# Kernel optimization log

Hardware: AMD Instinct MI355X
Metric: run time of the kernel (lower is better)

## Reference

```python
import jax, jax.numpy as jnp
import numpy as np

N = 50000      # nodes
E = 600000     # edges
D = 128        # hidden_dim (bottleneck=1)
G = 64         # graphs in batch
GN_EPS = 1e-5  # GraphNorm eps


def setup_inputs() -> dict:
    key = jax.random.key(0)
    ks = jax.random.split(key, 10)
    node_h = jax.random.normal(ks[0], (N, D), dtype=jnp.float32)
    edge_attr = jax.random.normal(ks[1], (E, D), dtype=jnp.float32)
    batch = jnp.sort(jax.random.randint(ks[2], (N,), 0, G)).astype(jnp.int64)
    edge_index = jax.random.randint(ks[3], (2, E), 0, N).astype(jnp.int64)
    # params: lin1, conv.lin (edge linear), conv.eps, GraphNorm(weight,bias,mean_scale)
    w1 = jax.random.normal(ks[4], (D, D), dtype=jnp.float32) * 0.02
    b1 = jnp.zeros((D,), dtype=jnp.float32)
    we = jax.random.normal(ks[5], (D, D), dtype=jnp.float32) * 0.02
    be = jnp.zeros((D,), dtype=jnp.float32)
    eps = jnp.zeros((), dtype=jnp.float32)  # train_eps, init 0
    gn_weight = jnp.ones((D,), dtype=jnp.float32)
    gn_bias = jnp.zeros((D,), dtype=jnp.float32)
    gn_mean_scale = jnp.ones((D,), dtype=jnp.float32)
    return {"node_h": node_h, "edge_attr": edge_attr, "batch": batch,
            "edge_index": edge_index, "w1": w1, "b1": b1, "we": we, "be": be,
            "eps": eps, "gn_weight": gn_weight, "gn_bias": gn_bias,
            "gn_mean_scale": gn_mean_scale}


def graph_norm(x, batch, weight, bias, mean_scale):
    ones = jnp.ones((x.shape[0],), dtype=x.dtype)
    cnt = jnp.maximum(jax.ops.segment_sum(ones, batch, num_segments=G), 1.0)[:, None]
    mean = jax.ops.segment_sum(x, batch, num_segments=G) / cnt
    out = x - mean[batch] * mean_scale
    var = jax.ops.segment_sum(out * out, batch, num_segments=G) / cnt
    std = jnp.sqrt(var + GN_EPS)
    return weight * out / std[batch] + bias


def reference(node_h, edge_attr, batch, edge_index, w1, b1, we, be, eps,
              gn_weight, gn_bias, gn_mean_scale):
    h = node_h @ w1.T + b1                                  # lin1: [N, D]
    src, dst = edge_index[0], edge_index[1]
    # GINEConvMod message: SiLU(x_j + lin(edge_attr)); gather -> add -> act
    msg = jax.nn.silu(h[src] + (edge_attr @ we.T + be))     # [E, D]
    agg = jax.ops.segment_sum(msg, dst, num_segments=N)     # scatter-add
    conv = (1.0 + eps) * h + agg                            # nn = Identity
    # dropout(p=0) and lin2=Identity are no-ops
    out = jax.nn.silu(conv)
    return graph_norm(out + node_h, batch, gn_weight, gn_bias, gn_mean_scale)
```

## Files before the change

kernel.cpp:

```cpp
#include <hip/hip_runtime.h>
#include <hip/hip_bf16.h>

#define NN 50000
#define NE 600000
#define DIM 128
#define NG 64
#define NCHUNK 98

using bf16x8 = __attribute__((ext_vector_type(8))) __bf16;
using f32x4  = __attribute__((ext_vector_type(4))) float;

__device__ __forceinline__ bf16x8 cvt8(const float* __restrict__ p) {
    f32x4 a = *(const f32x4*)p;
    f32x4 b = *(const f32x4*)(p + 4);
    bf16x8 r;
    #pragma unroll
    for (int i = 0; i < 4; ++i) { r[i] = (__bf16)a[i]; r[i + 4] = (__bf16)b[i]; }
    return r;
}

__device__ __forceinline__ void stage_weights(const float* __restrict__ W, __bf16* sW) {
    for (int i = threadIdx.x; i < 128 * 16; i += 256) {
        int row = i >> 4, seg = i & 15;
        *(bf16x8*)(&sW[row * 136 + seg * 8]) = cvt8(W + row * 128 + seg * 8);
    }
    __syncthreads();
}

__global__ __launch_bounds__(256) void gemm_bias(
    const float* __restrict__ X, const float* __restrict__ W,
    const float* __restrict__ bias, float* __restrict__ Y, int M)
{
    __shared__ __bf16 sW[128 * 136];
    stage_weights(W, sW);

    int wave = threadIdx.x >> 6, lane = threadIdx.x & 63;
    int col = lane & 15, quad = lane >> 4;
    int tile = (blockIdx.x * 4 + wave) * 16;
    if (tile >= M) return;

    f32x4 acc[8] = {};
    const float* xp = X + (size_t)(tile + col) * DIM + quad * 8;
    #pragma unroll
    for (int k0 = 0; k0 < 128; k0 += 32) {
        bf16x8 a = cvt8(xp + k0);
        #pragma unroll
        for (int t = 0; t < 8; ++t) {
            bf16x8 b = *(const bf16x8*)(&sW[(t * 16 + col) * 136 + k0 + quad * 8]);
            acc[t] = __builtin_amdgcn_mfma_f32_16x16x32_bf16(a, b, acc[t], 0, 0, 0);
        }
    }
    float bv[8];
    #pragma unroll
    for (int t = 0; t < 8; ++t) bv[t] = bias[t * 16 + col];
    #pragma unroll
    for (int r = 0; r < 4; ++r) {
        float* yp = Y + (size_t)(tile + quad * 4 + r) * DIM;
        #pragma unroll
        for (int t = 0; t < 8; ++t) yp[t * 16 + col] = acc[t][r] + bv[t];
    }
}

__global__ __launch_bounds__(256) void k_hist(const int* __restrict__ dst, int* __restrict__ deg) {
    int e = blockIdx.x * 256 + threadIdx.x;
    if (e < NE) atomicAdd(&deg[dst[e]], 1);
}

__global__ __launch_bounds__(256) void k_scan_a(const int* __restrict__ deg, int* __restrict__ chunkSum) {
    __shared__ int s[256];
    int c = blockIdx.x, t = threadIdx.x;
    int b = c * 512 + t;
    int v = (b < NN) ? deg[b] : 0;
    if (b + 256 < NN) v += deg[b + 256];
    s[t] = v; __syncthreads();
    for (int off = 128; off > 0; off >>= 1) {
        if (t < off) s[t] += s[t + off];
        __syncthreads();
    }
    if (t == 0) chunkSum[c] = s[0];
}

__global__ __launch_bounds__(128) void k_scan_b(const int* __restrict__ chunkSum,
                                                int* __restrict__ chunkOff, int* __restrict__ rowptr) {
    __shared__ int s[128];
    int t = threadIdx.x;
    int v = (t < NCHUNK) ? chunkSum[t] : 0;
    s[t] = v; __syncthreads();
    for (int off = 1; off < 128; off <<= 1) {
        int x = (t >= off) ? s[t - off] : 0;
        __syncthreads();
        s[t] += x;
        __syncthreads();
    }
    chunkOff[t] = s[t] - v;
    if (t == 0) rowptr[NN] = NE;
}

__global__ __launch_bounds__(512) void k_scan_c(const int* __restrict__ deg,
                                                const int* __restrict__ chunkOff,
                                                int* __restrict__ rowptr, int* __restrict__ pos) {
    __shared__ int s[512];
    int c = blockIdx.x, t = threadIdx.x;
    int i = c * 512 + t;
    int v = (i < NN) ? deg[i] : 0;
    s[t] = v; __syncthreads();
    for (int off = 1; off < 512; off <<= 1) {
        int x = (t >= off) ? s[t - off] : 0;
        __syncthreads();
        s[t] += x;
        __syncthreads();
    }
    if (i < NN) { rowptr[i] = chunkOff[c] + s[t] - v; pos[i] = 0; }
}

__global__ __launch_bounds__(256) void k_slot(const int* __restrict__ dst,
                                              const int* __restrict__ rowptr,
                                              int* __restrict__ pos, int* __restrict__ slot) {
    int e = blockIdx.x * 256 + threadIdx.x;
    if (e >= NE) return;
    int d = dst[e];
    int p = atomicAdd(&pos[d], 1);
    slot[e] = rowptr[d] + p;
}

__global__ __launch_bounds__(256) void edge_msg_sorted(
    const float* __restrict__ EA, const float* __restrict__ W,
    const float* __restrict__ bias,
    const int* __restrict__ src, const int* __restrict__ slot,
    const float* __restrict__ H, __hip_bfloat16* __restrict__ MSG)
{
    __shared__ __bf16 sW[128 * 136];
    stage_weights(W, sW);

    int wave = threadIdx.x >> 6, lane = threadIdx.x & 63;
    int col = lane & 15, quad = lane >> 4;
    int tile = (blockIdx.x * 4 + wave) * 16;

    f32x4 acc[8] = {};
    const float* xp = EA + (size_t)(tile + col) * DIM + quad * 8;
    #pragma unroll
    for (int k0 = 0; k0 < 128; k0 += 32) {
        bf16x8 a = cvt8(xp + k0);
        #pragma unroll
        for (int t = 0; t < 8; ++t) {
            bf16x8 b = *(const bf16x8*)(&sW[(t * 16 + col) * 136 + k0 + quad * 8]);
            acc[t] = __builtin_amdgcn_mfma_f32_16x16x32_bf16(a, b, acc[t], 0, 0, 0);
        }
    }
    float bv[8];
    #pragma unroll
    for (int t = 0; t < 8; ++t) bv[t] = bias[t * 16 + col];

    #pragma unroll
    for (int r = 0; r < 4; ++r) {
        int e = tile + quad * 4 + r;
        int s  = src[e];
        int sl = slot[e];
        const float* hp = H + (size_t)s * DIM;
        __hip_bfloat16* mp = MSG + (size_t)sl * DIM;
        #pragma unroll
        for (int t = 0; t < 8; ++t) {
            int d = t * 16 + col;
            float v = acc[t][r] + bv[t] + hp[d];
            v = v / (1.f + __expf(-v));
            mp[d] = __float2bfloat16(v);
        }
    }
}

__global__ __launch_bounds__(128) void k_gather(
    const __hip_bfloat16* __restrict__ MSG, const int* __restrict__ rowptr,
    float* __restrict__ H, const float* __restrict__ node_h,
    const float* __restrict__ epsp)
{
    int n = blockIdx.x, d = threadIdx.x;
    int s = rowptr[n], epos = rowptr[n + 1];
    float acc = 0.f;
    for (int e = s; e < epos; ++e)
        acc += __bfloat162float(MSG[(size_t)e * DIM + d]);
    size_t idx = (size_t)n * DIM + d;
    float v = (1.f + epsp[0]) * H[idx] + acc;
    v = v / (1.f + __expf(-v));
    H[idx] = v + node_h[idx];
}

__global__ __launch_bounds__(128) void stats_pass(
    const float* __restrict__ X, const int* __restrict__ batch,
    float* __restrict__ SUMS, float* __restrict__ CNT, int npb)
{
    int d = threadIdx.x;
    int n0 = blockIdx.x * npb;
    int nend = min(n0 + npb, NN);
    if (n0 >= NN) return;
    int cur_g = batch[n0];
    float run = 0.f; int runlen = 0;
    for (int n = n0; n < nend; ++n) {
        int g = batch[n];
        if (g != cur_g) {
            atomicAdd(&SUMS[cur_g * DIM + d], run);
            if (d == 0) atomicAdd(&CNT[cur_g], (float)runlen);
            run = 0.f; runlen = 0; cur_g = g;
        }
        run += X[(size_t)n * DIM + d]; runlen++;
    }
    atomicAdd(&SUMS[cur_g * DIM + d], run);
    if (d == 0) atomicAdd(&CNT[cur_g], (float)runlen);
}

__global__ __launch_bounds__(128) void var_pass(
    const float* __restrict__ X, const int* __restrict__ batch,
    const float* __restrict__ msc,
    const float* __restrict__ SUMS, const float* __restrict__ CNT,
    float* __restrict__ VARS, int npb)
{
    int d = threadIdx.x;
    int n0 = blockIdx.x * npb;
    int nend = min(n0 + npb, NN);
    if (n0 >= NN) return;
    float ms = msc[d];
    int cur_g = batch[n0];
    float c = fmaxf(CNT[cur_g], 1.f);
    float mean = SUMS[cur_g * DIM + d] / c;
    float run = 0.f;
    for (int n = n0; n < nend; ++n) {
        int g = batch[n];
        if (g != cur_g) {
            atomicAdd(&VARS[cur_g * DIM + d], run);
            run = 0.f; cur_g = g;
            c = fmaxf(CNT[g], 1.f);
            mean = SUMS[g * DIM + d] / c;
        }
        float v = X[(size_t)n * DIM + d] - mean * ms;
        run += v * v;
    }
    atomicAdd(&VARS[cur_g * DIM + d], run);
}

__global__ __launch_bounds__(128) void finalize(
    const float* __restrict__ X, const int* __restrict__ batch,
    const float* __restrict__ msc,
    const float* __restrict__ SUMS, const float* __restrict__ VARS,
    const float* __restrict__ CNT,
    const float* __restrict__ gw, const float* __restrict__ gb,
    float* __restrict__ OUT, int npb)
{
    int d = threadIdx.x;
    int n0 = blockIdx.x * npb;
    int nend = min(n0 + npb, NN);
    if (n0 >= NN) return;
    float ms = msc[d], wd = gw[d], bd = gb[d];
    int cur_g = -1;
    float mean = 0.f, rstd = 0.f;
    for (int n = n0; n < nend; ++n) {
        int g = batch[n];
        if (g != cur_g) {
            cur_g = g;
            float c = fmaxf(CNT[g], 1.f);
            mean = SUMS[g * DIM + d] / c;
            rstd = rsqrtf(VARS[g * DIM + d] / c + 1e-5f);
        }
        size_t idx = (size_t)n * DIM + d;
        float v = X[idx] - mean * ms;
        OUT[idx] = wd * v * rstd + bd;
    }
}

__global__ __launch_bounds__(256) void edge_msg_atomic(
    const float* __restrict__ EA, const float* __restrict__ W,
    const float* __restrict__ bias,
    const int* __restrict__ src, const int* __restrict__ dst,
    const float* __restrict__ H, float* __restrict__ AGG)
{
    __shared__ __bf16 sW[128 * 136];
    stage_weights(W, sW);
    int wave = threadIdx.x >> 6, lane = threadIdx.x & 63;
    int col = lane & 15, quad = lane >> 4;
    int tile = (blockIdx.x * 4 + wave) * 16;
    f32x4 acc[8] = {};
    const float* xp = EA + (size_t)(tile + col) * DIM + quad * 8;
    #pragma unroll
    for (int k0 = 0; k0 < 128; k0 += 32) {
        bf16x8 a = cvt8(xp + k0);
        #pragma unroll
        for (int t = 0; t < 8; ++t) {
            bf16x8 b = *(const bf16x8*)(&sW[(t * 16 + col) * 136 + k0 + quad * 8]);
            acc[t] = __builtin_amdgcn_mfma_f32_16x16x32_bf16(a, b, acc[t], 0, 0, 0);
        }
    }
    float bv[8];
    #pragma unroll
    for (int t = 0; t < 8; ++t) bv[t] = bias[t * 16 + col];
    #pragma unroll
    for (int r = 0; r < 4; ++r) {
        int e = tile + quad * 4 + r;
        int s = src[e], dd = dst[e];
        const float* hp = H + (size_t)s * DIM;
        float* ap = AGG + (size_t)dd * DIM;
        #pragma unroll
        for (int t = 0; t < 8; ++t) {
            int d = t * 16 + col;
            float v = acc[t][r] + bv[t] + hp[d];
            v = v / (1.f + __expf(-v));
            atomicAdd(&ap[d], v);
        }
    }
}

__global__ __launch_bounds__(128) void fuse_x_atomic(
    float* __restrict__ H, const float* __restrict__ AGG,
    const float* __restrict__ node_h, const float* __restrict__ epsp, int npb)
{
    int d = threadIdx.x;
    int n0 = blockIdx.x * npb;
    int nend = min(n0 + npb, NN);
    if (n0 >= NN) return;
    float epsv = 1.f + epsp[0];
    for (int n = n0; n < nend; ++n) {
        size_t idx = (size_t)n * DIM + d;
        float v = epsv * H[idx] + AGG[idx];
        v = v / (1.f + __expf(-v));
        H[idx] = v + node_h[idx];
    }
}

extern "C" void kernel_launch(void* const* d_in, const int* in_sizes, int n_in,
                              void* d_out, int out_size, void* d_ws, size_t ws_size,
                              hipStream_t stream) {
    const float* node_h    = (const float*)d_in[0];
    const float* edge_attr = (const float*)d_in[1];
    const int*   batch     = (const int*)d_in[2];
    const int*   eidx      = (const int*)d_in[3];
    const float* w1        = (const float*)d_in[4];
    const float* b1        = (const float*)d_in[5];
    const float* we        = (const float*)d_in[6];
    const float* be        = (const float*)d_in[7];
    const float* eps       = (const float*)d_in[8];
    const float* gnw       = (const float*)d_in[9];
    const float* gnb       = (const float*)d_in[10];
    const float* gnms      = (const float*)d_in[11];
    const int* src = eidx, * dst = eidx + NE;

    char* base = (char*)d_ws;
    float* H = (float*)base;

    size_t oMSG   = 25600000;
    size_t oROW   = oMSG + 153600000;
    size_t oDEG   = oROW + 200064;
    size_t oSUMS  = oDEG + 200000;
    size_t oVARS  = oSUMS + 32768;
    size_t oCNT   = oVARS + 32768;
    size_t oSLOT  = oCNT + 256;
    size_t oCSA   = oSLOT + 2400000;
    size_t oCSB   = oCSA + 512;
    size_t needed = oCSB + 512;

    bool fast = ws_size >= needed;

    if (fast) {
        __hip_bfloat16* MSG = (__hip_bfloat16*)(base + oMSG);
        int* rowptr = (int*)(base + oROW);
        int* deg    = (int*)(base + oDEG);
        float* SUMS = (float*)(base + oSUMS);
        float* VARS = (float*)(base + oVARS);
        float* CNT  = (float*)(base + oCNT);
        int* slot   = (int*)(base + oSLOT);
        int* csum   = (int*)(base + oCSA);
        int* coff   = (int*)(base + oCSB);

        hipMemsetAsync(deg, 0, 200000 + 32768 + 32768 + 256, stream);

        gemm_bias<<<782, 256, 0, stream>>>(node_h, w1, b1, H, NN);
        k_hist  <<<(NE + 255) / 256, 256, 0, stream>>>(dst, deg);
        k_scan_a<<<NCHUNK, 256, 0, stream>>>(deg, csum);
        k_scan_b<<<1, 128, 0, stream>>>(csum, coff, rowptr);
        k_scan_c<<<NCHUNK, 512, 0, stream>>>(deg, coff, rowptr, deg );
        k_slot  <<<(NE + 255) / 256, 256, 0, stream>>>(dst, rowptr, deg, slot);
        edge_msg_sorted<<<9375, 256, 0, stream>>>(edge_attr, we, be, src, slot, H, MSG);
        k_gather<<<NN, 128, 0, stream>>>(MSG, rowptr, H, node_h, eps);
        stats_pass<<<3125, 128, 0, stream>>>(H, batch, SUMS, CNT, 16);
        var_pass  <<<3125, 128, 0, stream>>>(H, batch, gnms, SUMS, CNT, VARS, 16);
        finalize  <<<3125, 128, 0, stream>>>(H, batch, gnms, SUMS, VARS, CNT, gnw, gnb,
                                             (float*)d_out, 16);
    } else {
        float* AGG  = H + 6400000;
        float* SUMS = H + 12800000;
        float* VARS = SUMS + NG * DIM;
        float* CNT  = VARS + NG * DIM;
        hipMemsetAsync(AGG, 0, (size_t)(6400000 + NG * DIM * 2 + NG) * sizeof(float), stream);
        gemm_bias<<<782, 256, 0, stream>>>(node_h, w1, b1, H, NN);
        edge_msg_atomic<<<9375, 256, 0, stream>>>(edge_attr, we, be, src, dst, H, AGG);
        fuse_x_atomic<<<3125, 128, 0, stream>>>(H, AGG, node_h, eps, 16);
        stats_pass<<<3125, 128, 0, stream>>>(H, batch, SUMS, CNT, 16);
        var_pass  <<<3125, 128, 0, stream>>>(H, batch, gnms, SUMS, CNT, VARS, 16);
        finalize  <<<3125, 128, 0, stream>>>(H, batch, gnms, SUMS, VARS, CNT, gnw, gnb,
                                             (float*)d_out, 16);
    }
}
```

Measured before the change: 725.9 us.

## Transpose MFMA operands for row-contiguous epilogues and fuse GraphNorm variance pass

Swaps the A/B operands of the MFMA so each lane holds four contiguous output columns of one row. Epilogues can then use vectorized f32x4 bias and H loads and f32x4 or bf16x4 stores, with one src/slot lookup per lane instead of four scattered ones. The gather loop is unrolled by four with independent accumulators. GraphNorm variance now comes from a single-pass sum of squares, E[x^2] - mean^2*ms*(2-ms), which drops one full read of H but is less numerically robust than the two-pass form.

```diff
diff --git a/kernel.cpp b/kernel.cpp
--- a/kernel.cpp
+++ b/kernel.cpp
@@ -8,6 +8,7 @@
 #define NCHUNK 98
 
 using bf16x8 = __attribute__((ext_vector_type(8))) __bf16;
+using bf16x4 = __attribute__((ext_vector_type(4))) __bf16;
 using f32x4  = __attribute__((ext_vector_type(4))) float;
 
 __device__ __forceinline__ bf16x8 cvt8(const float* __restrict__ p) {
@@ -43,21 +44,21 @@
     const float* xp = X + (size_t)(tile + col) * DIM + quad * 8;
     #pragma unroll
     for (int k0 = 0; k0 < 128; k0 += 32) {
-        bf16x8 a = cvt8(xp + k0);
+        bf16x8 b = cvt8(xp + k0);
         #pragma unroll
         for (int t = 0; t < 8; ++t) {
-            bf16x8 b = *(const bf16x8*)(&sW[(t * 16 + col) * 136 + k0 + quad * 8]);
+            bf16x8 a = *(const bf16x8*)(&sW[(t * 16 + col) * 136 + k0 + quad * 8]);
             acc[t] = __builtin_amdgcn_mfma_f32_16x16x32_bf16(a, b, acc[t], 0, 0, 0);
         }
     }
-    float bv[8];
-    #pragma unroll
-    for (int t = 0; t < 8; ++t) bv[t] = bias[t * 16 + col];
-    #pragma unroll
-    for (int r = 0; r < 4; ++r) {
-        float* yp = Y + (size_t)(tile + quad * 4 + r) * DIM;
-        #pragma unroll
-        for (int t = 0; t < 8; ++t) yp[t * 16 + col] = acc[t][r] + bv[t];
+    float* yp = Y + (size_t)(tile + col) * DIM + quad * 4;
+    #pragma unroll
+    for (int t = 0; t < 8; ++t) {
+        f32x4 bv = *(const f32x4*)(bias + t * 16 + quad * 4);
+        f32x4 o;
+        #pragma unroll
+        for (int r = 0; r < 4; ++r) o[r] = acc[t][r] + bv[r];
+        *(f32x4*)(yp + t * 16) = o;
     }
 }
 
@@ -140,31 +141,31 @@
     const float* xp = EA + (size_t)(tile + col) * DIM + quad * 8;
     #pragma unroll
     for (int k0 = 0; k0 < 128; k0 += 32) {
-        bf16x8 a = cvt8(xp + k0);
+        bf16x8 b = cvt8(xp + k0);
         #pragma unroll
         for (int t = 0; t < 8; ++t) {
-            bf16x8 b = *(const bf16x8*)(&sW[(t * 16 + col) * 136 + k0 + quad * 8]);
+            bf16x8 a = *(const bf16x8*)(&sW[(t * 16 + col) * 136 + k0 + quad * 8]);
             acc[t] = __builtin_amdgcn_mfma_f32_16x16x32_bf16(a, b, acc[t], 0, 0, 0);
         }
     }
-    float bv[8];
-    #pragma unroll
-    for (int t = 0; t < 8; ++t) bv[t] = bias[t * 16 + col];
-
-    #pragma unroll
-    for (int r = 0; r < 4; ++r) {
-        int e = tile + quad * 4 + r;
-        int s  = src[e];
-        int sl = slot[e];
-        const float* hp = H + (size_t)s * DIM;
-        __hip_bfloat16* mp = MSG + (size_t)sl * DIM;
-        #pragma unroll
-        for (int t = 0; t < 8; ++t) {
-            int d = t * 16 + col;
-            float v = acc[t][r] + bv[t] + hp[d];
+
+    int e  = tile + col;
+    int s  = src[e];
+    int sl = slot[e];
+    const float* hp = H + (size_t)s * DIM + quad * 4;
+    __hip_bfloat16* mp = MSG + (size_t)sl * DIM + quad * 4;
+    #pragma unroll
+    for (int t = 0; t < 8; ++t) {
+        f32x4 bv = *(const f32x4*)(bias + t * 16 + quad * 4);
+        f32x4 hv = *(const f32x4*)(hp + t * 16);
+        bf16x4 o;
+        #pragma unroll
+        for (int r = 0; r < 4; ++r) {
+            float v = acc[t][r] + bv[r] + hv[r];
             v = v / (1.f + __expf(-v));
-            mp[d] = __float2bfloat16(v);
-        }
+            o[r] = (__bf16)v;
+        }
+        *(bf16x4*)(mp + t * 16) = o;
     }
 }
 
@@ -175,9 +176,17 @@
 {
     int n = blockIdx.x, d = threadIdx.x;
     int s = rowptr[n], epos = rowptr[n + 1];
-    float acc = 0.f;
-    for (int e = s; e < epos; ++e)
-        acc += __bfloat162float(MSG[(size_t)e * DIM + d]);
+    const __hip_bfloat16* mp = MSG + (size_t)s * DIM + d;
+    float a0 = 0.f, a1 = 0.f, a2 = 0.f, a3 = 0.f;
+    int e = s;
+    for (; e + 4 <= epos; e += 4, mp += 4 * DIM) {
+        a0 += __bfloat162float(mp[0]);
+        a1 += __bfloat162float(mp[DIM]);
+        a2 += __bfloat162float(mp[2 * DIM]);
+        a3 += __bfloat162float(mp[3 * DIM]);
+    }
+    for (; e < epos; ++e, mp += DIM) a0 += __bfloat162float(mp[0]);
+    float acc = (a0 + a1) + (a2 + a3);
     size_t idx = (size_t)n * DIM + d;
     float v = (1.f + epsp[0]) * H[idx] + acc;
     v = v / (1.f + __expf(-v));
@@ -186,60 +195,35 @@
 
 __global__ __launch_bounds__(128) void stats_pass(
     const float* __restrict__ X, const int* __restrict__ batch,
-    float* __restrict__ SUMS, float* __restrict__ CNT, int npb)
+    float* __restrict__ SUMS, float* __restrict__ SQS,
+    float* __restrict__ CNT, int npb)
 {
     int d = threadIdx.x;
     int n0 = blockIdx.x * npb;
     int nend = min(n0 + npb, NN);
     if (n0 >= NN) return;
     int cur_g = batch[n0];
-    float run = 0.f; int runlen = 0;
+    float run = 0.f, run2 = 0.f; int runlen = 0;
     for (int n = n0; n < nend; ++n) {
         int g = batch[n];
         if (g != cur_g) {
             atomicAdd(&SUMS[cur_g * DIM + d], run);
+            atomicAdd(&SQS[cur_g * DIM + d], run2);
             if (d == 0) atomicAdd(&CNT[cur_g], (float)runlen);
-            run = 0.f; runlen = 0; cur_g = g;
-        }
-        run += X[(size_t)n * DIM + d]; runlen++;
+            run = 0.f; run2 = 0.f; runlen = 0; cur_g = g;
+        }
+        float x = X[(size_t)n * DIM + d];
+        run += x; run2 += x * x; runlen++;
     }
     atomicAdd(&SUMS[cur_g * DIM + d], run);
+    atomicAdd(&SQS[cur_g * DIM + d], run2);
     if (d == 0) atomicAdd(&CNT[cur_g], (float)runlen);
-}
-
-__global__ __launch_bounds__(128) void var_pass(
-    const float* __restrict__ X, const int* __restrict__ batch,
-    const float* __restrict__ msc,
-    const float* __restrict__ SUMS, const float* __restrict__ CNT,
-    float* __restrict__ VARS, int npb)
-{
-    int d = threadIdx.x;
-    int n0 = blockIdx.x * npb;
-    int nend = min(n0 + npb, NN);
-    if (n0 >= NN) return;
-    float ms = msc[d];
-    int cur_g = batch[n0];
-    float c = fmaxf(CNT[cur_g], 1.f);
-    float mean = SUMS[cur_g * DIM + d] / c;
-    float run = 0.f;
-    for (int n = n0; n < nend; ++n) {
-        int g = batch[n];
-        if (g != cur_g) {
-            atomicAdd(&VARS[cur_g * DIM + d], run);
-            run = 0.f; cur_g = g;
-            c = fmaxf(CNT[g], 1.f);
-            mean = SUMS[g * DIM + d] / c;
-        }
-        float v = X[(size_t)n * DIM + d] - mean * ms;
-        run += v * v;
-    }
-    atomicAdd(&VARS[cur_g * DIM + d], run);
 }
 
 __global__ __launch_bounds__(128) void finalize(
     const float* __restrict__ X, const int* __restrict__ batch,
     const float* __restrict__ msc,
-    const float* __restrict__ SUMS, const float* __restrict__ VARS,
+    const float* __restrict__ SUMS, const float* __restrict__ SQS,
     const float* __restrict__ CNT,
     const float* __restrict__ gw, const float* __restrict__ gb,
     float* __restrict__ OUT, int npb)
@@ -257,7 +241,9 @@
             cur_g = g;
             float c = fmaxf(CNT[g], 1.f);
             mean = SUMS[g * DIM + d] / c;
-            rstd = rsqrtf(VARS[g * DIM + d] / c + 1e-5f);
+            float ex2 = SQS[g * DIM + d] / c;
+            float var = ex2 - mean * mean * ms * (2.f - ms);
+            rstd = rsqrtf(fmaxf(var, 0.f) + 1e-5f);
         }
         size_t idx = (size_t)n * DIM + d;
         float v = X[idx] - mean * ms;
@@ -280,28 +266,26 @@
     const float* xp = EA + (size_t)(tile + col) * DIM + quad * 8;
     #pragma unroll
     for (int k0 = 0; k0 < 128; k0 += 32) {
-        bf16x8 a = cvt8(xp + k0);
+        bf16x8 b = cvt8(xp + k0);
         #pragma unroll
         for (int t = 0; t < 8; ++t) {
-            bf16x8 b = *(const bf16x8*)(&sW[(t * 16 + col) * 136 + k0 + quad * 8]);
+            bf16x8 a = *(const bf16x8*)(&sW[(t * 16 + col) * 136 + k0 + quad * 8]);
             acc[t] = __builtin_amdgcn_mfma_f32_16x16x32_bf16(a, b, acc[t], 0, 0, 0);
         }
     }
-    float bv[8];
-    #pragma unroll
-    for (int t = 0; t < 8; ++t) bv[t] = bias[t * 16 + col];
-    #pragma unroll
-    for (int r = 0; r < 4; ++r) {
-        int e = tile + quad * 4 + r;
-        int s = src[e], dd = dst[e];
-        const float* hp = H + (size_t)s * DIM;
-        float* ap = AGG + (size_t)dd * DIM;
-        #pragma unroll
-        for (int t = 0; t < 8; ++t) {
-            int d = t * 16 + col;
-            float v = acc[t][r] + bv[t] + hp[d];
+    int e = tile + col;
+    int s = src[e], dd = dst[e];
+    const float* hp = H + (size_t)s * DIM + quad * 4;
+    float* ap = AGG + (size_t)dd * DIM + quad * 4;
+    #pragma unroll
+    for (int t = 0; t < 8; ++t) {
+        f32x4 bv = *(const f32x4*)(bias + t * 16 + quad * 4);
+        f32x4 hv = *(const f32x4*)(hp + t * 16);
+        #pragma unroll
+        for (int r = 0; r < 4; ++r) {
+            float v = acc[t][r] + bv[r] + hv[r];
             v = v / (1.f + __expf(-v));
-            atomicAdd(&ap[d], v);
+            atomicAdd(&ap[t * 16 + r], v);
         }
     }
 }
@@ -347,8 +331,8 @@
     size_t oROW   = oMSG + 153600000;
     size_t oDEG   = oROW + 200064;
     size_t oSUMS  = oDEG + 200000;
-    size_t oVARS  = oSUMS + 32768;
-    size_t oCNT   = oVARS + 32768;
+    size_t oSQS   = oSUMS + 32768;
+    size_t oCNT   = oSQS + 32768;
     size_t oSLOT  = oCNT + 256;
     size_t oCSA   = oSLOT + 2400000;
     size_t oCSB   = oCSA + 512;
@@ -361,7 +345,7 @@
         int* rowptr = (int*)(base + oROW);
         int* deg    = (int*)(base + oDEG);
         float* SUMS = (float*)(base + oSUMS);
-        float* VARS = (float*)(base + oVARS);
+        float* SQS  = (float*)(base + oSQS);
         float* CNT  = (float*)(base + oCNT);
         int* slot   = (int*)(base + oSLOT);
         int* csum   = (int*)(base + oCSA);
@@ -377,22 +361,20 @@
         k_slot  <<<(NE + 255) / 256, 256, 0, stream>>>(dst, rowptr, deg, slot);
         edge_msg_sorted<<<9375, 256, 0, stream>>>(edge_attr, we, be, src, slot, H, MSG);
         k_gather<<<NN, 128, 0, stream>>>(MSG, rowptr, H, node_h, eps);
-        stats_pass<<<3125, 128, 0, stream>>>(H, batch, SUMS, CNT, 16);
-        var_pass  <<<3125, 128, 0, stream>>>(H, batch, gnms, SUMS, CNT, VARS, 16);
-        finalize  <<<3125, 128, 0, stream>>>(H, batch, gnms, SUMS, VARS, CNT, gnw, gnb,
+        stats_pass<<<3125, 128, 0, stream>>>(H, batch, SUMS, SQS, CNT, 16);
+        finalize  <<<3125, 128, 0, stream>>>(H, batch, gnms, SUMS, SQS, CNT, gnw, gnb,
                                              (float*)d_out, 16);
     } else {
         float* AGG  = H + 6400000;
         float* SUMS = H + 12800000;
-        float* VARS = SUMS + NG * DIM;
-        float* CNT  = VARS + NG * DIM;
+        float* SQS  = SUMS + NG * DIM;
+        float* CNT  = SQS + NG * DIM;
         hipMemsetAsync(AGG, 0, (size_t)(6400000 + NG * DIM * 2 + NG) * sizeof(float), stream);
         gemm_bias<<<782, 256, 0, stream>>>(node_h, w1, b1, H, NN);
         edge_msg_atomic<<<9375, 256, 0, stream>>>(edge_attr, we, be, src, dst, H, AGG);
         fuse_x_atomic<<<3125, 128, 0, stream>>>(H, AGG, node_h, eps, 16);
-        stats_pass<<<3125, 128, 0, stream>>>(H, batch, SUMS, CNT, 16);
-        var_pass  <<<3125, 128, 0, stream>>>(H, batch, gnms, SUMS, CNT, VARS, 16);
-        finalize  <<<3125, 128, 0, stream>>>(H, batch, gnms, SUMS, VARS, CNT, gnw, gnb,
+        stats_pass<<<3125, 128, 0, stream>>>(H, batch, SUMS, SQS, CNT, 16);
+        finalize  <<<3125, 128, 0, stream>>>(H, batch, gnms, SUMS, SQS, CNT, gnw, gnb,
                                              (float*)d_out, 16);
     }
 }
```

Result: faster. 699.9 us (-3.6%).
